# Performance work log

Hardware: AMD Instinct MI355X
Metric: run time of the kernel (lower is better)

Reference implementation:

```python
import jax, jax.numpy as jnp
import numpy as np

E = 512
H = 8
D = E // H
WIN = 128  # mask_window_size


def setup_inputs() -> dict:
    key = jax.random.key(0)
    k1, k2, k3, k4, k5 = jax.random.split(key, 5)
    B, L = 2, 4096
    s = 1.0 / np.sqrt(E)
    return {
        "x": jax.random.normal(k1, (B, L, E), dtype=jnp.float32),
        "in_proj_w": jax.random.normal(k2, (3 * E, E), dtype=jnp.float32) * s,
        "in_proj_b": jax.random.normal(k3, (3 * E,), dtype=jnp.float32) * 0.02,
        "out_w": jax.random.normal(k4, (E, E), dtype=jnp.float32) * s,
        "out_b": jax.random.normal(k5, (E,), dtype=jnp.float32) * 0.02,
    }


def reference(x, in_proj_w, in_proj_b, out_w, out_b):
    B, L, _ = x.shape
    # fused qkv projection (torch MultiheadAttention in_proj): x @ W.T + b
    qkv = jnp.einsum("ble,fe->blf", x, in_proj_w) + in_proj_b  # [B,L,3E]
    q, k, v = jnp.split(qkv, 3, axis=-1)
    # [B,H,L,D]
    q = q.reshape(B, L, H, D).transpose(0, 2, 1, 3)
    k = k.reshape(B, L, H, D).transpose(0, 2, 1, 3)
    v = v.reshape(B, L, H, D).transpose(0, 2, 1, 3)
    scores = jnp.einsum("bhqd,bhkd->bhqk", q, k) / jnp.sqrt(jnp.float32(D))
    # (diagonal stays blocked — faithful to the original gen_mask quirk)
    idx = jnp.arange(L)
    dist = jnp.abs(idx[:, None] - idx[None, :])
    blocked = (dist > WIN) | (dist == 0)  # [L,L]
    scores = jnp.where(blocked[None, None], -jnp.inf, scores)
    attn = jax.nn.softmax(scores, axis=-1)  # [B,H,L,L]
    out = jnp.einsum("bhqk,bhkd->bhqd", attn, v)  # [B,H,L,D]
    out = out.transpose(0, 2, 1, 3).reshape(B, L, E)
    return jnp.einsum("ble,fe->blf", out, out_w) + out_b
```

## Files before the change

### kernel.cpp

```cpp
#include <hip/hip_runtime.h>
#include <math.h>

#define E_DIM 512
#define H_DIM 8
#define WIN 128
#define L_SEQ 4096
#define B_SZ 2

typedef unsigned short ushort_t;
typedef unsigned int uint_t;
typedef __attribute__((ext_vector_type(8))) __bf16 bf16x8;
typedef __attribute__((ext_vector_type(4))) float f32x4;

__device__ __forceinline__ ushort_t f2bf(float f) {
    uint_t u = __float_as_uint(f);
    u = u + 0x7fffu + ((u >> 16) & 1u);
    return (ushort_t)(u >> 16);
}
__device__ __forceinline__ uint_t pk2bf(float lo, float hi) {
    uint_t r;
    asm("v_cvt_pk_bf16_f32 %0, %1, %2" : "=v"(r) : "v"(lo), "v"(hi));
    return r;
}

__device__ __forceinline__ void gload16(const ushort_t* g, ushort_t* l) {
    __builtin_amdgcn_global_load_lds(
        (const __attribute__((address_space(1))) void*)g,
        (__attribute__((address_space(3))) void*)l,
        16, 0, 0);
}


__global__ __launch_bounds__(256) void convertX(
    const float* __restrict__ x,  ushort_t* __restrict__ xh,
    const float* __restrict__ w1, ushort_t* __restrict__ w1h,
    const float* __restrict__ w2, ushort_t* __restrict__ w2h) {
    int sg = blockIdx.x * 256 + threadIdx.x;
    const float* src; ushort_t* dh;
    if (sg < 524288)      { src = x;  dh = xh; }
    else if (sg < 622592) { src = w1; dh = w1h; sg -= 524288; }
    else                  { src = w2; dh = w2h; sg -= 622592; }
    const int tile = sg >> 6, slot = sg & 63;
    const int row = (tile >> 4) * 16 + (slot & 15);
    const int k   = (tile & 15) * 32 + (slot >> 4) * 8;
    const float4 v0 = *(const float4*)&src[(size_t)row * 512 + k];
    const float4 v1 = *(const float4*)&src[(size_t)row * 512 + k + 4];
    uint4 ov;
    ov.x = pk2bf(v0.x, v0.y);
    ov.y = pk2bf(v0.z, v0.w);
    ov.z = pk2bf(v1.x, v1.y);
    ov.w = pk2bf(v1.z, v1.w);
    *(uint4*)(dh + (size_t)sg * 8) = ov;
}

__global__ __launch_bounds__(256) void gemm_qkv(
    const ushort_t* __restrict__ Ah,
    const ushort_t* __restrict__ Wh,
    const float* __restrict__ bias,
    ushort_t* __restrict__ qTh,
    ushort_t* __restrict__ kTh,
    ushort_t* __restrict__ vTh) {
    __shared__ __align__(16) ushort_t sAh[3][8 * 512];
    __shared__ __align__(16) ushort_t sWh[3][8 * 512];

    const int tid = threadIdx.x, lane = tid & 63, w = tid >> 6;
    const int wm = w & 1, wn = w >> 1, ln = lane & 15, quad = lane >> 4;
    const int bx = blockIdx.x, by = blockIdx.y;
    const int lo8 = lane * 8;
    const int wu = __builtin_amdgcn_readfirstlane(w);

    const ushort_t* sA0 = &sAh[0][0];
    const ushort_t* sW0 = &sWh[0][0];
    const int BUF = 8 * 512;

    f32x4 acc[4][4];
    const f32x4 zero = {0.f, 0.f, 0.f, 0.f};
    #pragma unroll
    for (int i = 0; i < 4; i++)
        #pragma unroll
        for (int j = 0; j < 4; j++) acc[i][j] = zero;

    const ushort_t* pb[4];
    ushort_t* db[4];
    #pragma unroll
    for (int t = 0; t < 4; t++) {
        const int g = wu * 4 + t;
        if (g < 8) {
            pb[t] = Ah + ((size_t)(bx * 8 + g) * 16) * 512;
            db[t] = &sAh[0][g * 512];
        } else {
            const int u = g - 8;
            pb[t] = Wh + ((size_t)(by * 8 + u) * 16) * 512;
            db[t] = &sWh[0][u * 512];
        }
    }

    #pragma unroll
    for (int t = 0; t < 4; t++) gload16(pb[t] + lo8, db[t]);
    #pragma unroll
    for (int t = 0; t < 4; t++) gload16(pb[t] + 512 + lo8, db[t] + BUF);

    int bw = 2, br = 0;
    for (int kt = 0; kt < 16; kt++) {
        if (kt < 15) asm volatile("s_waitcnt vmcnt(4) lgkmcnt(0)" ::: "memory");
        else         asm volatile("s_waitcnt vmcnt(0) lgkmcnt(0)" ::: "memory");
        __builtin_amdgcn_s_barrier();
        __builtin_amdgcn_sched_barrier(0);

        if (kt < 14) {
            const int koff = (kt + 2) * 512;
            const int bwo = bw * BUF;
            #pragma unroll
            for (int t = 0; t < 4; t++)
                gload16(pb[t] + koff + lo8, db[t] + bwo);
            bw = (bw == 2) ? 0 : bw + 1;
        }

        const int bro = br * BUF;
        br = (br == 2) ? 0 : br + 1;

        bf16x8 fah[4];
        #pragma unroll
        for (int i = 0; i < 4; i++)
            fah[i] = *(const bf16x8*)&sA0[bro + (wm * 4 + i) * 512 + lo8];
        #pragma unroll
        for (int j = 0; j < 4; j++) {
            const bf16x8 fbh = *(const bf16x8*)&sW0[bro + (wn * 4 + j) * 512 + lo8];
            #pragma unroll
            for (int i = 0; i < 4; i++)
                acc[i][j] = __builtin_amdgcn_mfma_f32_16x16x32_bf16(fah[i], fbh, acc[i][j], 0, 0, 0);
        }
    }

    const int b = bx >> 5;
    const int h = 2 * (by & 3) + wn;
    if (by < 8) {
        ushort_t* dh = (by < 4) ? qTh : kTh;
        #pragma unroll
        for (int i = 0; i < 4; i++) {
            const int rt = (bx & 31) * 8 + wm * 4 + i;
            const size_t tb = ((size_t)(b * 8 + h) * 256 + rt) * 2;
            #pragma unroll
            for (int j = 0; j < 4; j++) {
                const float bv = bias[by * 128 + wn * 64 + j * 16 + ln];
                const size_t tile = tb + (j >> 1);
                const uint_t pa = pk2bf(acc[i][j][0] + bv, acc[i][j][1] + bv);
                const uint_t pc = pk2bf(acc[i][j][2] + bv, acc[i][j][3] + bv);
                const int slot0 = ((j * 2 + (ln >> 3)) & 3) * 16 + quad * 4;
                const size_t idx0 = tile * 512 + slot0 * 8 + (ln & 7);
                dh[idx0]      = (ushort_t)pa;
                dh[idx0 + 8]  = (ushort_t)(pa >> 16);
                dh[idx0 + 16] = (ushort_t)pc;
                dh[idx0 + 24] = (ushort_t)(pc >> 16);
            }
        }
    } else {
        const int kwin = (bx & 31) * 2 + wm;
        #pragma unroll
        for (int i = 0; i < 4; i++) {
            const int kk = i >> 1;
            #pragma unroll
            for (int j = 0; j < 4; j++) {
                const float bv = bias[by * 128 + wn * 64 + j * 16 + ln];
                const size_t tile = (((size_t)(b * 8 + h) * 64 + kwin) * 4 + j) * 2 + kk;
                const uint_t pa = pk2bf(acc[i][j][0] + bv, acc[i][j][1] + bv);
                const uint_t pc = pk2bf(acc[i][j][2] + bv, acc[i][j][3] + bv);
                const int slot = ((i & 1) * 2 + (quad >> 1)) * 16 + ln;
                uint2 ov; ov.x = pa; ov.y = pc;
                *(uint2*)&vTh[tile * 512 + slot * 8 + (quad & 1) * 4] = ov;
            }
        }
    }
}

__global__ __launch_bounds__(512) void attn_mfma(
    const ushort_t* __restrict__ qTh,
    const ushort_t* __restrict__ kTh,
    const ushort_t* __restrict__ vTh,
    ushort_t* __restrict__ outh) {
    __shared__ __align__(16) ushort_t sKh[3][8 * 512];
    __shared__ __align__(16) ushort_t sV [3][8 * 512];
    __shared__ __align__(16) ushort_t sP [16 * 512];

    const int qs = blockIdx.x * 128;
    const int h = blockIdx.y, b = blockIdx.z;
    const int bh = b * 8 + h;
    const int tid = threadIdx.x, lane = tid & 63;
    const int w = tid >> 6, ln = lane & 15, quad = lane >> 4;
    const int lo8 = lane * 8;

    bf16x8 qf[2];
    {
        const size_t qt = ((size_t)bh * 256 + (qs >> 4) + w) * 2;
        qf[0] = *(const bf16x8*)(qTh + (qt + 0) * 512 + lo8);
        qf[1] = *(const bf16x8*)(qTh + (qt + 1) * 512 + lo8);
    }

    f32x4 oacc[4];
    const f32x4 zero = {0.f, 0.f, 0.f, 0.f};
    #pragma unroll
    for (int dt = 0; dt < 4; dt++) oacc[dt] = zero;
    float m_run = -1e30f, l_loc = 0.f;

    const float cscale = 0.125f * 1.44269504f;
    const int qlo = qs + 16 * w;
    const int q = qlo + ln;
    const int lo_b = (q - WIN) < 0 ? 0 : (q - WIN);
    const int hi_b = (q + WIN) > (L_SEQ - 1) ? (L_SEQ - 1) : (q + WIN);

    auto stage = [&](int t, int bi) {
        if (w < 4) {
            int st = (qs >> 4) - 8 + t * 4 + w;
            st = st < 0 ? 0 : (st > 255 ? 255 : st);
            const size_t kb = ((size_t)bh * 256 + st) * 2 * 512 + lo8;
            gload16(kTh + kb,       &sKh[bi][(w * 2 + 0) * 512]);
            gload16(kTh + kb + 512, &sKh[bi][(w * 2 + 1) * 512]);
        } else {
            const int u = w - 4;
            int vw = (qs >> 6) - 2 + t;
            vw = vw < 0 ? 0 : (vw > 63 ? 63 : vw);
            const size_t vb = (((size_t)bh * 64 + vw) * 4 + u) * 2 * 512 + lo8;
            gload16(vTh + vb,       &sV[bi][(u * 2 + 0) * 512]);
            gload16(vTh + vb + 512, &sV[bi][(u * 2 + 1) * 512]);
        }
    };

    stage(0, 0);
    stage(1, 1);

    #pragma unroll
    for (int kt = 0; kt < 6; kt++) {
        const int ks = qs - 128 + kt * 64;

        if (kt < 5) asm volatile("s_waitcnt vmcnt(2) lgkmcnt(0)" ::: "memory");
        else        asm volatile("s_waitcnt vmcnt(0) lgkmcnt(0)" ::: "memory");
        __builtin_amdgcn_s_barrier();
        __builtin_amdgcn_sched_barrier(0);

        if (kt < 4) stage(kt + 2, (kt + 2) % 3);
        const int cb = kt % 3;

        bool dead[4];
        #pragma unroll
        for (int jt = 0; jt < 4; jt++) {
            const int klo = ks + 16 * jt;
            dead[jt] = (klo > qlo + 15 + WIN) || (klo + 15 < qlo - WIN) ||
                       (klo >= L_SEQ) || (klo + 15 < 0);
        }
        const bool hdead0 = dead[0] && dead[1];
        const bool hdead1 = dead[2] && dead[3];
        const bool ktAlive = !(hdead0 && hdead1);

        if (ktAlive) {
            f32x4 st4[4];
            __builtin_amdgcn_s_setprio(1);
            #pragma unroll
            for (int jt = 0; jt < 4; jt++) {
                f32x4 a = zero;
                if (!dead[jt]) {
                    #pragma unroll
                    for (int kk = 0; kk < 2; kk++) {
                        const bf16x8 kh = *(const bf16x8*)&sKh[cb][(jt * 2 + kk) * 512 + lo8];
                        a = __builtin_amdgcn_mfma_f32_16x16x32_bf16(kh, qf[kk], a, 0, 0, 0);
                    }
                }
                st4[jt] = a;
            }
            __builtin_amdgcn_s_setprio(0);

            float lmax = -INFINITY;
            #pragma unroll
            for (int jt = 0; jt < 4; jt++)
                if (!dead[jt])
                    #pragma unroll
                    for (int r = 0; r < 4; r++)
                        lmax = fmaxf(lmax, st4[jt][r]);

            const bool trig = __any(lmax * cscale > m_run + 8.f);
            if (trig) {
                float mk = fmaxf(lmax, __shfl_xor(lmax, 16));
                mk = fmaxf(mk, __shfl_xor(mk, 32));
                const float mnew = fmaxf(m_run, mk * cscale);
                const float alpha = exp2f(m_run - mnew);
                m_run = mnew;
                l_loc *= alpha;
                float ar[4];
                #pragma unroll
                for (int r = 0; r < 4; r++)
                    ar[r] = __shfl(alpha, quad * 4 + r);
                #pragma unroll
                for (int dt = 0; dt < 4; dt++)
                    #pragma unroll
                    for (int r = 0; r < 4; r++)
                        oacc[dt][r] *= ar[r];
            }

            #pragma unroll
            for (int jt = 0; jt < 4; jt++) {
                if (!dead[jt]) {
                    #pragma unroll
                    for (int r = 0; r < 4; r++) {
                        const int kcol = ks + jt * 16 + quad * 4 + r;
                        const bool ok = (kcol >= lo_b) && (kcol <= hi_b) && (kcol != q);
                        float p = exp2f(st4[jt][r] * cscale - m_run);
                        p = ok ? p : 0.f;
                        st4[jt][r] = p;
                        l_loc += p;
                    }
                }
            }

            #pragma unroll
            for (int jt = 0; jt < 4; jt++) {
                const bool hd = (jt < 2) ? hdead0 : hdead1;
                if (!hd) {
                    uint2 pw;
                    if (!dead[jt]) {
                        pw.x = pk2bf(st4[jt][0], st4[jt][1]);
                        pw.y = pk2bf(st4[jt][2], st4[jt][3]);
                    } else { pw.x = 0u; pw.y = 0u; }
                    const int slot = ((jt & 1) * 2 + (quad >> 1)) * 16 + ln;
                    *(uint2*)&sP[w * 1024 + (jt >> 1) * 512 + slot * 8 + (quad & 1) * 4] = pw;
                }
            }

            #pragma unroll
            for (int kk = 0; kk < 2; kk++) {
                const bool hd = (kk == 0) ? hdead0 : hdead1;
                if (!hd) {
                    const bf16x8 pf = *(const bf16x8*)&sP[w * 1024 + kk * 512 + lo8];
                    __builtin_amdgcn_s_setprio(1);
                    #pragma unroll
                    for (int dt = 0; dt < 4; dt++) {
                        const bf16x8 vf = *(const bf16x8*)&sV[cb][(dt * 2 + kk) * 512 + lo8];
                        oacc[dt] = __builtin_amdgcn_mfma_f32_16x16x32_bf16(pf, vf, oacc[dt], 0, 0, 0);
                    }
                    __builtin_amdgcn_s_setprio(0);
                }
            }
        }
    }

    float ls = l_loc;
    ls += __shfl_xor(ls, 16);
    ls += __shfl_xor(ls, 32);
    const int Rt = ((b * L_SEQ + qs) >> 4) + w;
    float invl[4];
    #pragma unroll
    for (int r = 0; r < 4; r++) {
        const float lr = __shfl(ls, quad * 4 + r);
        invl[r] = __builtin_amdgcn_rcpf(lr);
    }
    #pragma unroll
    for (int dt = 0; dt < 4; dt++) {
        const uint_t pa = pk2bf(oacc[dt][0] * invl[0], oacc[dt][1] * invl[1]);
        const uint_t pc = pk2bf(oacc[dt][2] * invl[2], oacc[dt][3] * invl[3]);
        const int tile = Rt * 16 + h * 2 + (dt >> 1);
        const int slot0 = ((dt & 1) * 2 + (ln >> 3)) * 16 + quad * 4;
        const size_t idx0 = (size_t)tile * 512 + slot0 * 8 + (ln & 7);
        outh[idx0]      = (ushort_t)pa;
        outh[idx0 + 8]  = (ushort_t)(pa >> 16);
        outh[idx0 + 16] = (ushort_t)pc;
        outh[idx0 + 24] = (ushort_t)(pc >> 16);
    }
}

__global__ __launch_bounds__(512) void gemm_out(
    const ushort_t* __restrict__ Ah,
    const ushort_t* __restrict__ Wh,
    const float* __restrict__ bias, float* __restrict__ C) {
    __shared__ __align__(16) ushort_t sAh[3][16 * 512];
    __shared__ __align__(16) ushort_t sWh[3][8 * 512];

    const int tid = threadIdx.x, lane = tid & 63, w = tid >> 6;
    const int wm = w & 3, wn = w >> 2, ln = lane & 15, quad = lane >> 4;
    const int bx = blockIdx.x, by = blockIdx.y;
    const int lo8 = lane * 8;
    const int wu = __builtin_amdgcn_readfirstlane(w);

    const ushort_t* sA0 = &sAh[0][0];
    const ushort_t* sW0 = &sWh[0][0];
    const int BUFA = 16 * 512, BUFW = 8 * 512;

    f32x4 acc[2][2];
    const f32x4 zero = {0.f, 0.f, 0.f, 0.f};
    #pragma unroll
    for (int i = 0; i < 2; i++)
        #pragma unroll
        for (int j = 0; j < 2; j++) acc[i][j] = zero;

    const ushort_t* pb[3];
    ushort_t* db[3];
    int ds[3];
    #pragma unroll
    for (int t = 0; t < 3; t++) {
        const int g = wu * 3 + t;
        if (g < 16) {
            pb[t] = Ah + ((size_t)(bx * 8 + (g >> 1)) * 16 + (g & 1)) * 512;
            db[t] = &sAh[0][g * 512]; ds[t] = BUFA;
        } else {
            const int u = g - 16;
            pb[t] = Wh + ((size_t)(by * 4 + (u >> 1)) * 16 + (u & 1)) * 512;
            db[t] = &sWh[0][u * 512]; ds[t] = BUFW;
        }
    }

    #pragma unroll
    for (int t = 0; t < 3; t++) gload16(pb[t] + lo8, db[t]);
    #pragma unroll
    for (int t = 0; t < 3; t++) gload16(pb[t] + 1024 + lo8, db[t] + ds[t]);

    int bw = 2, br = 0;
    for (int KT = 0; KT < 8; KT++) {
        if (KT < 7) asm volatile("s_waitcnt vmcnt(3) lgkmcnt(0)" ::: "memory");
        else        asm volatile("s_waitcnt vmcnt(0) lgkmcnt(0)" ::: "memory");
        __builtin_amdgcn_s_barrier();
        __builtin_amdgcn_sched_barrier(0);

        if (KT < 6) {
            const int koff = (KT + 2) * 1024;
            #pragma unroll
            for (int t = 0; t < 3; t++)
                gload16(pb[t] + koff + lo8, db[t] + bw * ds[t]);
            bw = (bw == 2) ? 0 : bw + 1;
        }

        const int broA = br * BUFA, broW = br * BUFW;
        br = (br == 2) ? 0 : br + 1;

        #pragma unroll
        for (int ks = 0; ks < 2; ks++) {
            bf16x8 fah[2];
            #pragma unroll
            for (int i = 0; i < 2; i++)
                fah[i] = *(const bf16x8*)&sA0[broA + ((wm * 2 + i) * 2 + ks) * 512 + lo8];
            #pragma unroll
            for (int j = 0; j < 2; j++) {
                const bf16x8 fbh = *(const bf16x8*)&sW0[broW + ((wn * 2 + j) * 2 + ks) * 512 + lo8];
                #pragma unroll
                for (int i = 0; i < 2; i++)
                    acc[i][j] = __builtin_amdgcn_mfma_f32_16x16x32_bf16(fah[i], fbh, acc[i][j], 0, 0, 0);
            }
        }
    }

    #pragma unroll
    for (int i = 0; i < 2; i++) {
        const int row0 = bx * 128 + wm * 32 + i * 16 + quad * 4;
        #pragma unroll
        for (int j = 0; j < 2; j++) {
            const int col = by * 64 + wn * 32 + j * 16 + ln;
            const float bv = bias[col];
            #pragma unroll
            for (int r = 0; r < 4; r++)
                C[(size_t)(row0 + r) * E_DIM + col] = acc[i][j][r] + bv;
        }
    }
}

extern "C" void kernel_launch(void* const* d_in, const int* in_sizes, int n_in,
                              void* d_out, int out_size, void* d_ws, size_t ws_size,
                              hipStream_t stream) {
    const float* x         = (const float*)d_in[0];
    const float* in_proj_w = (const float*)d_in[1];
    const float* in_proj_b = (const float*)d_in[2];
    const float* out_w     = (const float*)d_in[3];
    const float* out_b     = (const float*)d_in[4];
    float* out = (float*)d_out;

    const int N = B_SZ * L_SEQ;
    const size_t NE = (size_t)N * E_DIM;

    char* p = (char*)d_ws;
    ushort_t* xh  = (ushort_t*)p; p += NE * 2;
    ushort_t* w1h = (ushort_t*)p; p += (size_t)3 * E_DIM * E_DIM * 2;
    ushort_t* w2h = (ushort_t*)p; p += (size_t)E_DIM * E_DIM * 2;
    ushort_t* qTh = (ushort_t*)p; p += NE * 2;
    ushort_t* kTh = (ushort_t*)p; p += NE * 2;
    ushort_t* vTh = (ushort_t*)p; p += NE * 2;
    ushort_t* ath = (ushort_t*)p; p += NE * 2;

    convertX<<<2560, 256, 0, stream>>>(x, xh, in_proj_w, w1h, out_w, w2h);

    gemm_qkv<<<dim3(64, 12), 256, 0, stream>>>(
        xh, w1h, in_proj_b, qTh, kTh, vTh);

    attn_mfma<<<dim3(L_SEQ / 128, H_DIM, B_SZ), 512, 0, stream>>>(
        qTh, kTh, vTh, ath);

    gemm_out<<<dim3(64, 8), 512, 0, stream>>>(
        ath, w2h, out_b, out);
}
```

Measured before the change: 126.6 us.

## Load GEMM MFMA fragments directly from global into registers, dropping LDS staging

Both the QKV and output projection GEMMs drop their triple-buffered LDS pipeline, barriers and waitcnt control. Each wave now loads its pre-tiled bf16 fragments straight from global memory into registers, double-buffered across k-steps, and feeds them to MFMA. This removes LDS traffic and block-wide synchronisation. In exchange, fragments shared by waves in a block are fetched repeatedly from global/L2 instead of once per block, and each wave has fewer loads in flight to hide latency.

```diff
diff --git a/kernel.cpp b/kernel.cpp
--- a/kernel.cpp
+++ b/kernel.cpp
@@ -60,18 +60,10 @@
     ushort_t* __restrict__ qTh,
     ushort_t* __restrict__ kTh,
     ushort_t* __restrict__ vTh) {
-    __shared__ __align__(16) ushort_t sAh[3][8 * 512];
-    __shared__ __align__(16) ushort_t sWh[3][8 * 512];
-
     const int tid = threadIdx.x, lane = tid & 63, w = tid >> 6;
     const int wm = w & 1, wn = w >> 1, ln = lane & 15, quad = lane >> 4;
     const int bx = blockIdx.x, by = blockIdx.y;
     const int lo8 = lane * 8;
-    const int wu = __builtin_amdgcn_readfirstlane(w);
-
-    const ushort_t* sA0 = &sAh[0][0];
-    const ushort_t* sW0 = &sWh[0][0];
-    const int BUF = 8 * 512;
 
     f32x4 acc[4][4];
     const f32x4 zero = {0.f, 0.f, 0.f, 0.f};
@@ -80,56 +72,39 @@
         #pragma unroll
         for (int j = 0; j < 4; j++) acc[i][j] = zero;
 
-    const ushort_t* pb[4];
-    ushort_t* db[4];
-    #pragma unroll
-    for (int t = 0; t < 4; t++) {
-        const int g = wu * 4 + t;
-        if (g < 8) {
-            pb[t] = Ah + ((size_t)(bx * 8 + g) * 16) * 512;
-            db[t] = &sAh[0][g * 512];
-        } else {
-            const int u = g - 8;
-            pb[t] = Wh + ((size_t)(by * 8 + u) * 16) * 512;
-            db[t] = &sWh[0][u * 512];
-        }
-    }
-
-    #pragma unroll
-    for (int t = 0; t < 4; t++) gload16(pb[t] + lo8, db[t]);
-    #pragma unroll
-    for (int t = 0; t < 4; t++) gload16(pb[t] + 512 + lo8, db[t] + BUF);
-
-    int bw = 2, br = 0;
-    for (int kt = 0; kt < 16; kt++) {
-        if (kt < 15) asm volatile("s_waitcnt vmcnt(4) lgkmcnt(0)" ::: "memory");
-        else         asm volatile("s_waitcnt vmcnt(0) lgkmcnt(0)" ::: "memory");
-        __builtin_amdgcn_s_barrier();
-        __builtin_amdgcn_sched_barrier(0);
-
-        if (kt < 14) {
-            const int koff = (kt + 2) * 512;
-            const int bwo = bw * BUF;
-            #pragma unroll
-            for (int t = 0; t < 4; t++)
-                gload16(pb[t] + koff + lo8, db[t] + bwo);
-            bw = (bw == 2) ? 0 : bw + 1;
-        }
-
-        const int bro = br * BUF;
-        br = (br == 2) ? 0 : br + 1;
-
-        bf16x8 fah[4];
-        #pragma unroll
-        for (int i = 0; i < 4; i++)
-            fah[i] = *(const bf16x8*)&sA0[bro + (wm * 4 + i) * 512 + lo8];
-        #pragma unroll
-        for (int j = 0; j < 4; j++) {
-            const bf16x8 fbh = *(const bf16x8*)&sW0[bro + (wn * 4 + j) * 512 + lo8];
+    const ushort_t* aB = Ah + ((size_t)(bx * 8 + wm * 4) * 16) * 512 + lo8;
+    const ushort_t* wB = Wh + ((size_t)(by * 8 + wn * 4) * 16) * 512 + lo8;
+
+    bf16x8 a0[4], b0[4], a1[4], b1[4];
+    #pragma unroll
+    for (int i = 0; i < 4; i++) {
+        a0[i] = *(const bf16x8*)(aB + (size_t)i * 8192);
+        b0[i] = *(const bf16x8*)(wB + (size_t)i * 8192);
+    }
+
+    for (int kt = 0; kt < 16; kt += 2) {
+        #pragma unroll
+        for (int i = 0; i < 4; i++) {
+            a1[i] = *(const bf16x8*)(aB + (size_t)i * 8192 + (kt + 1) * 512);
+            b1[i] = *(const bf16x8*)(wB + (size_t)i * 8192 + (kt + 1) * 512);
+        }
+        #pragma unroll
+        for (int j = 0; j < 4; j++)
             #pragma unroll
             for (int i = 0; i < 4; i++)
-                acc[i][j] = __builtin_amdgcn_mfma_f32_16x16x32_bf16(fah[i], fbh, acc[i][j], 0, 0, 0);
-        }
+                acc[i][j] = __builtin_amdgcn_mfma_f32_16x16x32_bf16(a0[i], b0[j], acc[i][j], 0, 0, 0);
+        if (kt + 2 < 16) {
+            #pragma unroll
+            for (int i = 0; i < 4; i++) {
+                a0[i] = *(const bf16x8*)(aB + (size_t)i * 8192 + (kt + 2) * 512);
+                b0[i] = *(const bf16x8*)(wB + (size_t)i * 8192 + (kt + 2) * 512);
+            }
+        }
+        #pragma unroll
+        for (int j = 0; j < 4; j++)
+            #pragma unroll
+            for (int i = 0; i < 4; i++)
+                acc[i][j] = __builtin_amdgcn_mfma_f32_16x16x32_bf16(a1[i], b1[j], acc[i][j], 0, 0, 0);
     }
 
     const int b = bx >> 5;
@@ -196,8 +171,8 @@
         qf[1] = *(const bf16x8*)(qTh + (qt + 1) * 512 + lo8);
     }
 
+    const f32x4 zero = {0.f, 0.f, 0.f, 0.f};
     f32x4 oacc[4];
-    const f32x4 zero = {0.f, 0.f, 0.f, 0.f};
     #pragma unroll
     for (int dt = 0; dt < 4; dt++) oacc[dt] = zero;
     float m_run = -1e30f, l_loc = 0.f;
@@ -369,18 +344,10 @@
     const ushort_t* __restrict__ Ah,
     const ushort_t* __restrict__ Wh,
     const float* __restrict__ bias, float* __restrict__ C) {
-    __shared__ __align__(16) ushort_t sAh[3][16 * 512];
-    __shared__ __align__(16) ushort_t sWh[3][8 * 512];
-
     const int tid = threadIdx.x, lane = tid & 63, w = tid >> 6;
     const int wm = w & 3, wn = w >> 2, ln = lane & 15, quad = lane >> 4;
     const int bx = blockIdx.x, by = blockIdx.y;
     const int lo8 = lane * 8;
-    const int wu = __builtin_amdgcn_readfirstlane(w);
-
-    const ushort_t* sA0 = &sAh[0][0];
-    const ushort_t* sW0 = &sWh[0][0];
-    const int BUFA = 16 * 512, BUFW = 8 * 512;
 
     f32x4 acc[2][2];
     const f32x4 zero = {0.f, 0.f, 0.f, 0.f};
@@ -389,59 +356,39 @@
         #pragma unroll
         for (int j = 0; j < 2; j++) acc[i][j] = zero;
 
-    const ushort_t* pb[3];
-    ushort_t* db[3];
-    int ds[3];
-    #pragma unroll
-    for (int t = 0; t < 3; t++) {
-        const int g = wu * 3 + t;
-        if (g < 16) {
-            pb[t] = Ah + ((size_t)(bx * 8 + (g >> 1)) * 16 + (g & 1)) * 512;
-            db[t] = &sAh[0][g * 512]; ds[t] = BUFA;
-        } else {
-            const int u = g - 16;
-            pb[t] = Wh + ((size_t)(by * 4 + (u >> 1)) * 16 + (u & 1)) * 512;
-            db[t] = &sWh[0][u * 512]; ds[t] = BUFW;
-        }
-    }
-
-    #pragma unroll
-    for (int t = 0; t < 3; t++) gload16(pb[t] + lo8, db[t]);
-    #pragma unroll
-    for (int t = 0; t < 3; t++) gload16(pb[t] + 1024 + lo8, db[t] + ds[t]);
-
-    int bw = 2, br = 0;
-    for (int KT = 0; KT < 8; KT++) {
-        if (KT < 7) asm volatile("s_waitcnt vmcnt(3) lgkmcnt(0)" ::: "memory");
-        else        asm volatile("s_waitcnt vmcnt(0) lgkmcnt(0)" ::: "memory");
-        __builtin_amdgcn_s_barrier();
-        __builtin_amdgcn_sched_barrier(0);
-
-        if (KT < 6) {
-            const int koff = (KT + 2) * 1024;
-            #pragma unroll
-            for (int t = 0; t < 3; t++)
-                gload16(pb[t] + koff + lo8, db[t] + bw * ds[t]);
-            bw = (bw == 2) ? 0 : bw + 1;
-        }
-
-        const int broA = br * BUFA, broW = br * BUFW;
-        br = (br == 2) ? 0 : br + 1;
-
-        #pragma unroll
-        for (int ks = 0; ks < 2; ks++) {
-            bf16x8 fah[2];
+    const ushort_t* aB = Ah + ((size_t)(bx * 8 + wm * 2) * 16) * 512 + lo8;
+    const ushort_t* wB = Wh + ((size_t)(by * 4 + wn * 2) * 16) * 512 + lo8;
+
+    bf16x8 a0[2], b0[2], a1[2], b1[2];
+    #pragma unroll
+    for (int i = 0; i < 2; i++) {
+        a0[i] = *(const bf16x8*)(aB + (size_t)i * 8192);
+        b0[i] = *(const bf16x8*)(wB + (size_t)i * 8192);
+    }
+
+    for (int kt = 0; kt < 16; kt += 2) {
+        #pragma unroll
+        for (int i = 0; i < 2; i++) {
+            a1[i] = *(const bf16x8*)(aB + (size_t)i * 8192 + (kt + 1) * 512);
+            b1[i] = *(const bf16x8*)(wB + (size_t)i * 8192 + (kt + 1) * 512);
+        }
+        #pragma unroll
+        for (int j = 0; j < 2; j++)
             #pragma unroll
             for (int i = 0; i < 2; i++)
-                fah[i] = *(const bf16x8*)&sA0[broA + ((wm * 2 + i) * 2 + ks) * 512 + lo8];
-            #pragma unroll
-            for (int j = 0; j < 2; j++) {
-                const bf16x8 fbh = *(const bf16x8*)&sW0[broW + ((wn * 2 + j) * 2 + ks) * 512 + lo8];
-                #pragma unroll
-                for (int i = 0; i < 2; i++)
-                    acc[i][j] = __builtin_amdgcn_mfma_f32_16x16x32_bf16(fah[i], fbh, acc[i][j], 0, 0, 0);
-            }
-        }
+                acc[i][j] = __builtin_amdgcn_mfma_f32_16x16x32_bf16(a0[i], b0[j], acc[i][j], 0, 0, 0);
+        if (kt + 2 < 16) {
+            #pragma unroll
+            for (int i = 0; i < 2; i++) {
+                a0[i] = *(const bf16x8*)(aB + (size_t)i * 8192 + (kt + 2) * 512);
+                b0[i] = *(const bf16x8*)(wB + (size_t)i * 8192 + (kt + 2) * 512);
+            }
+        }
+        #pragma unroll
+        for (int j = 0; j < 2; j++)
+            #pragma unroll
+            for (int i = 0; i < 2; i++)
+                acc[i][j] = __builtin_amdgcn_mfma_f32_16x16x32_bf16(a1[i], b1[j], acc[i][j], 0, 0, 0);
     }
 
     #pragma unroll
```

Measured after the change: 147.8 us. +16.7%, slower.

## Fuse fp32-to-bf16 conversion of x into the QKV GEMM load pipeline

Applied to the files above, without the earlier changes.

The separate pass that converted x to bf16 is removed, and the conversion kernel now handles only the weights. In the QKV GEMM, two of the four warps load fp32 x directly into registers, convert it to bf16 and write it to LDS, using a register double-buffer. The other two warps keep the async global-to-LDS triple-buffered path for the weights. This drops a full read and write of x through HBM and one kernel's worth of work, at the cost of an uneven load split between warps and conversion work inside the GEMM main loop.

```diff
diff --git a/kernel.cpp b/kernel.cpp
--- a/kernel.cpp
+++ b/kernel.cpp
@@ -31,15 +31,13 @@
 }
 
 
-__global__ __launch_bounds__(256) void convertX(
-    const float* __restrict__ x,  ushort_t* __restrict__ xh,
+__global__ __launch_bounds__(256) void convertW(
     const float* __restrict__ w1, ushort_t* __restrict__ w1h,
     const float* __restrict__ w2, ushort_t* __restrict__ w2h) {
     int sg = blockIdx.x * 256 + threadIdx.x;
     const float* src; ushort_t* dh;
-    if (sg < 524288)      { src = x;  dh = xh; }
-    else if (sg < 622592) { src = w1; dh = w1h; sg -= 524288; }
-    else                  { src = w2; dh = w2h; sg -= 622592; }
+    if (sg < 98304) { src = w1; dh = w1h; }
+    else            { src = w2; dh = w2h; sg -= 98304; }
     const int tile = sg >> 6, slot = sg & 63;
     const int row = (tile >> 4) * 16 + (slot & 15);
     const int k   = (tile & 15) * 32 + (slot >> 4) * 8;
@@ -54,13 +52,13 @@
 }
 
 __global__ __launch_bounds__(256) void gemm_qkv(
-    const ushort_t* __restrict__ Ah,
+    const float* __restrict__ X,
     const ushort_t* __restrict__ Wh,
     const float* __restrict__ bias,
     ushort_t* __restrict__ qTh,
     ushort_t* __restrict__ kTh,
     ushort_t* __restrict__ vTh) {
-    __shared__ __align__(16) ushort_t sAh[3][8 * 512];
+    __shared__ __align__(16) ushort_t sAh[2][8 * 512];
     __shared__ __align__(16) ushort_t sWh[3][8 * 512];
 
     const int tid = threadIdx.x, lane = tid & 63, w = tid >> 6;
@@ -71,7 +69,7 @@
 
     const ushort_t* sA0 = &sAh[0][0];
     const ushort_t* sW0 = &sWh[0][0];
-    const int BUF = 8 * 512;
+    const int BUFA = 8 * 512, BUFW = 8 * 512;
 
     f32x4 acc[4][4];
     const f32x4 zero = {0.f, 0.f, 0.f, 0.f};
@@ -80,56 +78,114 @@
         #pragma unroll
         for (int j = 0; j < 4; j++) acc[i][j] = zero;
 
-    const ushort_t* pb[4];
-    ushort_t* db[4];
+    const float* xr[4];
+    ushort_t* adst[4];
+    const ushort_t* wp[4];
+    ushort_t* wdst[4];
     #pragma unroll
     for (int t = 0; t < 4; t++) {
-        const int g = wu * 4 + t;
-        if (g < 8) {
-            pb[t] = Ah + ((size_t)(bx * 8 + g) * 16) * 512;
-            db[t] = &sAh[0][g * 512];
+        if (wu < 2) {
+            const int g = wu * 4 + t;
+            xr[t] = X + ((size_t)((bx * 8 + g) * 16 + ln)) * 512 + quad * 8;
+            adst[t] = (ushort_t*)&sAh[0][g * 512 + lo8];
+            wp[t] = nullptr; wdst[t] = nullptr;
         } else {
-            const int u = g - 8;
-            pb[t] = Wh + ((size_t)(by * 8 + u) * 16) * 512;
-            db[t] = &sWh[0][u * 512];
-        }
-    }
-
-    #pragma unroll
-    for (int t = 0; t < 4; t++) gload16(pb[t] + lo8, db[t]);
-    #pragma unroll
-    for (int t = 0; t < 4; t++) gload16(pb[t] + 512 + lo8, db[t] + BUF);
-
-    int bw = 2, br = 0;
-    for (int kt = 0; kt < 16; kt++) {
-        if (kt < 15) asm volatile("s_waitcnt vmcnt(4) lgkmcnt(0)" ::: "memory");
-        else         asm volatile("s_waitcnt vmcnt(0) lgkmcnt(0)" ::: "memory");
+            const int u = (wu - 2) * 4 + t;
+            wp[t] = Wh + ((size_t)(by * 8 + u) * 16) * 512 + lo8;
+            wdst[t] = &sWh[0][u * 512];
+            xr[t] = nullptr; adst[t] = nullptr;
+        }
+    }
+
+    float4 P[4][2], Q[4][2];
+
+    if (wu < 2) {
+        #pragma unroll
+        for (int t = 0; t < 4; t++) {
+            P[t][0] = *(const float4*)(xr[t] + 0);
+            P[t][1] = *(const float4*)(xr[t] + 4);
+        }
+        #pragma unroll
+        for (int t = 0; t < 4; t++) {
+            Q[t][0] = *(const float4*)(xr[t] + 32);
+            Q[t][1] = *(const float4*)(xr[t] + 36);
+        }
+        #pragma unroll
+        for (int t = 0; t < 4; t++) {
+            uint4 ov;
+            ov.x = pk2bf(P[t][0].x, P[t][0].y);
+            ov.y = pk2bf(P[t][0].z, P[t][0].w);
+            ov.z = pk2bf(P[t][1].x, P[t][1].y);
+            ov.w = pk2bf(P[t][1].z, P[t][1].w);
+            *(uint4*)(adst[t]) = ov;
+        }
+    } else {
+        #pragma unroll
+        for (int t = 0; t < 4; t++) gload16(wp[t], wdst[t]);
+        #pragma unroll
+        for (int t = 0; t < 4; t++) gload16(wp[t] + 512, wdst[t] + BUFW);
+    }
+
+    auto iter = [&](int kt, float4 (&cur)[4][2], float4 (&nxt)[4][2]) {
+        if (wu < 2) {
+            asm volatile("s_waitcnt lgkmcnt(0)" ::: "memory");
+        } else {
+            if (kt < 15) asm volatile("s_waitcnt vmcnt(4) lgkmcnt(0)" ::: "memory");
+            else         asm volatile("s_waitcnt vmcnt(0) lgkmcnt(0)" ::: "memory");
+        }
         __builtin_amdgcn_s_barrier();
         __builtin_amdgcn_sched_barrier(0);
 
-        if (kt < 14) {
-            const int koff = (kt + 2) * 512;
-            const int bwo = bw * BUF;
-            #pragma unroll
-            for (int t = 0; t < 4; t++)
-                gload16(pb[t] + koff + lo8, db[t] + bwo);
-            bw = (bw == 2) ? 0 : bw + 1;
-        }
-
-        const int bro = br * BUF;
-        br = (br == 2) ? 0 : br + 1;
-
+        if (wu < 2) {
+            if (kt + 2 < 16) {
+                const int ko = (kt + 2) * 32;
+                #pragma unroll
+                for (int t = 0; t < 4; t++) {
+                    nxt[t][0] = *(const float4*)(xr[t] + ko);
+                    nxt[t][1] = *(const float4*)(xr[t] + ko + 4);
+                }
+            }
+            __builtin_amdgcn_sched_barrier(0);
+            if (kt + 1 < 16) {
+                const int bo = ((kt + 1) & 1) * BUFA;
+                #pragma unroll
+                for (int t = 0; t < 4; t++) {
+                    uint4 ov;
+                    ov.x = pk2bf(cur[t][0].x, cur[t][0].y);
+                    ov.y = pk2bf(cur[t][0].z, cur[t][0].w);
+                    ov.z = pk2bf(cur[t][1].x, cur[t][1].y);
+                    ov.w = pk2bf(cur[t][1].z, cur[t][1].w);
+                    *(uint4*)(adst[t] + bo) = ov;
+                }
+            }
+        } else {
+            if (kt + 2 < 16) {
+                const int ko = (kt + 2) * 512;
+                const int bo = ((kt + 2) % 3) * BUFW;
+                #pragma unroll
+                for (int t = 0; t < 4; t++)
+                    gload16(wp[t] + ko, wdst[t] + bo);
+            }
+        }
+
+        const int abuf = (kt & 1) * BUFA;
+        const int wbuf = (kt % 3) * BUFW;
         bf16x8 fah[4];
         #pragma unroll
         for (int i = 0; i < 4; i++)
-            fah[i] = *(const bf16x8*)&sA0[bro + (wm * 4 + i) * 512 + lo8];
+            fah[i] = *(const bf16x8*)&sA0[abuf + (wm * 4 + i) * 512 + lo8];
         #pragma unroll
         for (int j = 0; j < 4; j++) {
-            const bf16x8 fbh = *(const bf16x8*)&sW0[bro + (wn * 4 + j) * 512 + lo8];
+            const bf16x8 fbh = *(const bf16x8*)&sW0[wbuf + (wn * 4 + j) * 512 + lo8];
             #pragma unroll
             for (int i = 0; i < 4; i++)
                 acc[i][j] = __builtin_amdgcn_mfma_f32_16x16x32_bf16(fah[i], fbh, acc[i][j], 0, 0, 0);
         }
+    };
+
+    for (int kt2 = 0; kt2 < 16; kt2 += 2) {
+        iter(kt2,     Q, P);
+        iter(kt2 + 1, P, Q);
     }
 
     const int b = bx >> 5;
@@ -196,8 +252,8 @@
         qf[1] = *(const bf16x8*)(qTh + (qt + 1) * 512 + lo8);
     }
 
+    const f32x4 zero = {0.f, 0.f, 0.f, 0.f};
     f32x4 oacc[4];
-    const f32x4 zero = {0.f, 0.f, 0.f, 0.f};
     #pragma unroll
     for (int dt = 0; dt < 4; dt++) oacc[dt] = zero;
     float m_run = -1e30f, l_loc = 0.f;
@@ -479,11 +535,12 @@
     ushort_t* kTh = (ushort_t*)p; p += NE * 2;
     ushort_t* vTh = (ushort_t*)p; p += NE * 2;
     ushort_t* ath = (ushort_t*)p; p += NE * 2;
-
-    convertX<<<2560, 256, 0, stream>>>(x, xh, in_proj_w, w1h, out_w, w2h);
+    (void)xh;
+
+    convertW<<<512, 256, 0, stream>>>(in_proj_w, w1h, out_w, w2h);
 
     gemm_qkv<<<dim3(64, 12), 256, 0, stream>>>(
-        xh, w1h, in_proj_b, qTh, kTh, vTh);
+        x, w1h, in_proj_b, qTh, kTh, vTh);
 
     attn_mfma<<<dim3(L_SEQ / 128, H_DIM, B_SZ), 512, 0, stream>>>(
         qTh, kTh, vTh, ath);
```

Measured after the change: 147.2 us. +16.2%, slower.
